# Kernel tuning notes

Hardware: AMD Instinct MI355X
Metric: run time of the kernel (lower is better)

Reference implementation:

```python
import jax, jax.numpy as jnp
import numpy as np

NL, DM, DI, DS, DR, DC = 4, 1024, 2048, 16, 64, 4
B, L, DLOC, NC = 8, 224, 672, 10
EPS = 1e-5


def _rmsnorm(h, w):
    return h * jax.lax.rsqrt(jnp.mean(h * h, axis=-1, keepdims=True) + EPS) * w


def setup_inputs() -> dict:
    key = jax.random.key(0)
    ks = jax.random.split(key, 10)
    s = 0.02
    return dict(
        x=jax.random.normal(ks[0], (B, L, DLOC), jnp.float32),
        w_proj=jax.random.normal(ks[1], (DLOC, DM), jnp.float32) * s,
        b_proj=jnp.zeros((DM,), jnp.float32),
        norm_w=jnp.ones((NL, DM), jnp.float32),
        w_in=jax.random.normal(ks[2], (NL, DM, 2 * DI), jnp.float32) * s,
        w_conv=jax.random.normal(ks[3], (NL, DI, DC), jnp.float32) * s,
        b_conv=jnp.zeros((NL, DI), jnp.float32),
        w_x=jax.random.normal(ks[4], (NL, DI, DR + 2 * DS), jnp.float32) * s,
        w_dt=jax.random.normal(ks[5], (NL, DR, DI), jnp.float32) * s,
        b_dt=jax.random.normal(ks[6], (NL, DI), jnp.float32) * 0.1,
        A_log=jnp.broadcast_to(jnp.log(jnp.arange(1, DS + 1, dtype=jnp.float32)), (NL, DI, DS)) + jnp.zeros((NL, DI, DS), jnp.float32),
        Dp=jnp.ones((NL, DI), jnp.float32),
        w_out=jax.random.normal(ks[7], (NL, DI, DM), jnp.float32) * s,
        final_norm_w=jnp.ones((DM,), jnp.float32),
        w_fc=jax.random.normal(ks[8], (DM, NC), jnp.float32) * s,
        b_fc=jnp.zeros((NC,), jnp.float32),
    )


def reference(x, w_proj, b_proj, norm_w, w_in, w_conv, b_conv, w_x, w_dt, b_dt, A_log, Dp, w_out, final_norm_w, w_fc, b_fc):
    # input_proj: (B,L,DLOC) -> (B,L,DM)
    h = x @ w_proj + b_proj
    for l in range(NL):
        xn = _rmsnorm(h, norm_w[l])
        xz = xn @ w_in[l]                      # (B,L,2*DI)
        xp, z = jnp.split(xz, 2, axis=-1)
        # causal depthwise conv1d along L, kernel size DC
        xpad = jnp.pad(xp, ((0, 0), (DC - 1, 0), (0, 0)))
        xc = sum(xpad[:, k:k + L, :] * w_conv[l][:, k] for k in range(DC)) + b_conv[l]
        xc = jax.nn.silu(xc)
        x_dbl = xc @ w_x[l]                    # (B,L,DR+2*DS)
        dtr, Bm, Cm = jnp.split(x_dbl, [DR, DR + DS], axis=-1)
        dt = jax.nn.softplus(dtr @ w_dt[l] + b_dt[l])   # (B,L,DI)
        A = -jnp.exp(A_log[l])                 # (DI,DS)
        xs = (jnp.swapaxes(dt, 0, 1), jnp.swapaxes(Bm, 0, 1),
              jnp.swapaxes(Cm, 0, 1), jnp.swapaxes(xc, 0, 1))

        def step(hs, inp):
            dt_t, B_t, C_t, u_t = inp          # (B,DI),(B,DS),(B,DS),(B,DI)
            dA = jnp.exp(dt_t[:, :, None] * A)                        # (B,DI,DS)
            hs = dA * hs + (dt_t * u_t)[:, :, None] * B_t[:, None, :]
            y = jnp.einsum('bds,bs->bd', hs, C_t)
            return hs, y

        h0 = jnp.zeros((B, DI, DS), x.dtype)
        _, ys = jax.lax.scan(step, h0, xs)     # ys: (L,B,DI)
        y = jnp.swapaxes(ys, 0, 1) + Dp[l] * xc
        y = y * jax.nn.silu(z)
        h = h + y @ w_out[l]
    h = _rmsnorm(h, final_norm_w)
    pooled = h[:, -1, :]                       # last-token pooling
    return pooled @ w_fc + b_fc                # (B,NC)
```

## Files before the change

### kernel.cpp

```cpp
#include <hip/hip_runtime.h>
#include <hip/hip_bf16.h>
#include <hip/hip_fp16.h>
#include <math.h>

#define NL 4
#define DM 1024
#define DI 2048
#define DS 16
#define DR 64
#define DC 4
#define B_ 8
#define L_ 224
#define DLOC 672
#define NC 10
#define EPS 1e-5f

#define ROWS (B_ * L_)

typedef unsigned short u16;
typedef __attribute__((ext_vector_type(8))) short bf16x8;
typedef __attribute__((ext_vector_type(4))) float f32x4;
typedef __attribute__((address_space(1))) const void gvoid_t;
typedef __attribute__((address_space(3))) void lvoid_t;

__device__ __forceinline__ u16 f2bf(float f) {
  union { float f; unsigned int u; } v;
  v.f = f;
  unsigned int u = v.u;
  return (u16)((u + 0x7fffu + ((u >> 16) & 1u)) >> 16);
}

__device__ __forceinline__ void load4h(const __half* p, float* o) {
  uint2 r = *(const uint2*)p;
  __half2 h0 = *(__half2*)&r.x;
  __half2 h1 = *(__half2*)&r.y;
  float2 f0 = __half22float2(h0);
  float2 f1 = __half22float2(h1);
  o[0] = f0.x; o[1] = f0.y; o[2] = f1.x; o[3] = f1.y;
}

__device__ __forceinline__ void load8h(const __half* p, float* o) {
  uint4 r = *(const uint4*)p;
  __half2 h0 = *(__half2*)&r.x;
  __half2 h1 = *(__half2*)&r.y;
  __half2 h2 = *(__half2*)&r.z;
  __half2 h3 = *(__half2*)&r.w;
  float2 f0 = __half22float2(h0);
  float2 f1 = __half22float2(h1);
  float2 f2 = __half22float2(h2);
  float2 f3 = __half22float2(h3);
  o[0] = f0.x; o[1] = f0.y; o[2] = f1.x; o[3] = f1.y;
  o[4] = f2.x; o[5] = f2.y; o[6] = f3.x; o[7] = f3.y;
}

template <int ACC, int BIAS, int TSTORE>
__global__ __launch_bounds__(256) void gemm_bt_mfma(
    const u16* __restrict__ A, const u16* __restrict__ Bt,
    const float* __restrict__ bias, float* __restrict__ C, int K, int lda,
    int ldb, int ldc) {
  __shared__ __align__(16) u16 As[128 * 32];
  __shared__ __align__(16) u16 Bs[128 * 32];
  const int tid = threadIdx.x;
  const int lane = tid & 63;
  const int wv = tid >> 6;
  const int n0 = blockIdx.x * 128;
  const int m0 = blockIdx.y * 128;
  const int wm0 = (wv & 1) * 64;
  const int wn0 = (wv >> 1) * 64;
  const int quad = lane >> 4;
  const int l16 = lane & 15;

  const int srow = wv * 32 + (lane >> 2);
  const int scol = (lane & 3) * 8;
  const u16* ga0 = A + (size_t)(m0 + srow) * lda + scol;
  const u16* ga1 = ga0 + (size_t)16 * lda;
  const u16* gb0 = Bt + (size_t)(n0 + srow) * ldb + scol;
  const u16* gb1 = gb0 + (size_t)16 * ldb;
  u16* la0 = &As[(wv * 32) * 32];
  u16* la1 = &As[(wv * 32 + 16) * 32];
  u16* lb0 = &Bs[(wv * 32) * 32];
  u16* lb1 = &Bs[(wv * 32 + 16) * 32];

  f32x4 acc[4][4] = {};

  for (int k0 = 0; k0 < K; k0 += 32) {
    __syncthreads();
    __builtin_amdgcn_global_load_lds((gvoid_t*)ga0, (lvoid_t*)la0, 16, 0, 0);
    __builtin_amdgcn_global_load_lds((gvoid_t*)ga1, (lvoid_t*)la1, 16, 0, 0);
    __builtin_amdgcn_global_load_lds((gvoid_t*)gb0, (lvoid_t*)lb0, 16, 0, 0);
    __builtin_amdgcn_global_load_lds((gvoid_t*)gb1, (lvoid_t*)lb1, 16, 0, 0);
    __syncthreads();
    bf16x8 af[4], bfr[4];
#pragma unroll
    for (int i = 0; i < 4; i++)
      af[i] = *(const bf16x8*)&As[(wm0 + i * 16 + l16) * 32 + quad * 8];
#pragma unroll
    for (int j = 0; j < 4; j++)
      bfr[j] = *(const bf16x8*)&Bs[(wn0 + j * 16 + l16) * 32 + quad * 8];
#pragma unroll
    for (int i = 0; i < 4; i++)
#pragma unroll
      for (int j = 0; j < 4; j++)
        acc[i][j] = __builtin_amdgcn_mfma_f32_16x16x32_bf16(af[i], bfr[j],
                                                            acc[i][j], 0, 0, 0);
    ga0 += 32; ga1 += 32; gb0 += 32; gb1 += 32;
  }

#pragma unroll
  for (int i = 0; i < 4; i++) {
#pragma unroll
    for (int j = 0; j < 4; j++) {
      const int col = n0 + wn0 + j * 16 + l16;
      const int rowb = m0 + wm0 + i * 16 + quad * 4;
      if (TSTORE) {
        __half* Ch = (__half*)C;
        __half2 p0, p1;
        p0.x = __float2half(acc[i][j][0]); p0.y = __float2half(acc[i][j][1]);
        p1.x = __float2half(acc[i][j][2]); p1.y = __float2half(acc[i][j][3]);
        union { __half2 h[2]; uint2 u; } pk;
        pk.h[0] = p0; pk.h[1] = p1;
        *(uint2*)(Ch + (size_t)col * ldc + rowb) = pk.u;
      } else {
        float bv = 0.f;
        if (BIAS) bv = bias[col];
#pragma unroll
        for (int r = 0; r < 4; r++) {
          float v = acc[i][j][r] + bv;
          float* p = C + (size_t)(rowb + r) * ldc + col;
          if (ACC) v += *p;
          *p = v;
        }
      }
    }
  }
}

template <int ACC, int ACT, int SPLITK, int BROW, typename BT, typename OT>
__global__ __launch_bounds__(256) void gemm_kernel(
    const float* __restrict__ A, const BT* __restrict__ Bm,
    const float* __restrict__ bias, OT* __restrict__ C, int M, int N, int K,
    int lda, int ldb, int ldc) {
  if (SPLITK) {
    A += (size_t)blockIdx.z * 256;
    Bm += (size_t)blockIdx.z * 256 * ldb;
  }
  __shared__ float As[16][64];
  __shared__ float Bs[16][64];
  const int tid = threadIdx.x;
  const int tx = tid & 15;
  const int ty = tid >> 4;
  const int n0 = blockIdx.x * 64;
  const int m0 = blockIdx.y * 64;
  const int am = tid & 63;
  const int ak = (tid >> 6) * 4;
  const int bk = tid >> 4;
  const int bn = (tid & 15) * 4;

  float acc[4][4];
#pragma unroll
  for (int i = 0; i < 4; i++)
#pragma unroll
    for (int j = 0; j < 4; j++) acc[i][j] = 0.f;

  for (int k0 = 0; k0 < K; k0 += 16) {
    float4 av = *(const float4*)(A + (size_t)(m0 + am) * lda + k0 + ak);
    float4 bv;
    {
      int n = n0 + bn;
      const BT* bp = Bm + (size_t)(k0 + bk) * ldb + n;
      if (n + 3 < N) {
        if (sizeof(BT) == 2) {
          load4h((const __half*)bp, (float*)&bv);
        } else {
          bv = *(const float4*)(const void*)bp;
        }
      } else {
        bv.x = (n + 0 < N) ? (float)bp[0] : 0.f;
        bv.y = (n + 1 < N) ? (float)bp[1] : 0.f;
        bv.z = (n + 2 < N) ? (float)bp[2] : 0.f;
        bv.w = (n + 3 < N) ? (float)bp[3] : 0.f;
      }
    }
    __syncthreads();
    As[ak + 0][am] = av.x;
    As[ak + 1][am] = av.y;
    As[ak + 2][am] = av.z;
    As[ak + 3][am] = av.w;
    *(float4*)(&Bs[bk][bn]) = bv;
    __syncthreads();
#pragma unroll
    for (int kk = 0; kk < 16; kk++) {
      float4 a4 = *(const float4*)(&As[kk][ty * 4]);
      float4 b4 = *(const float4*)(&Bs[kk][tx * 4]);
      float ar[4] = {a4.x, a4.y, a4.z, a4.w};
      float br[4] = {b4.x, b4.y, b4.z, b4.w};
#pragma unroll
      for (int i = 0; i < 4; i++)
#pragma unroll
        for (int j = 0; j < 4; j++) acc[i][j] = fmaf(ar[i], br[j], acc[i][j]);
    }
  }

#pragma unroll
  for (int i = 0; i < 4; i++) {
    int m = m0 + ty * 4 + i;
#pragma unroll
    for (int j = 0; j < 4; j++) {
      int n = n0 + tx * 4 + j;
      if (n < N && m < M) {
        float v = acc[i][j];
        if (BROW == 2) v += bias[m];
        if (ACT == 1) v = (v > 20.f) ? v : log1pf(expf(v));
        OT* p = C + (size_t)m * ldc + n;
        if (ACC == 2) {
          atomicAdd((float*)p, v);
        } else {
          *p = (OT)v;
        }
      }
    }
  }
}

__global__ __launch_bounds__(256) void transpose_cvt_kernel(
    const float* __restrict__ src, u16* __restrict__ dst, int K, int N) {
  __shared__ float t[32][33];
  const int n0 = blockIdx.x * 32;
  const int k0 = blockIdx.y * 32;
  const int c = threadIdx.x & 31;
  const int r = threadIdx.x >> 5;
#pragma unroll
  for (int rr = 0; rr < 4; rr++)
    t[r + rr * 8][c] = src[(size_t)(k0 + r + rr * 8) * N + n0 + c];
  __syncthreads();
#pragma unroll
  for (int rr = 0; rr < 4; rr++)
    dst[(size_t)(n0 + r + rr * 8) * K + k0 + c] = f2bf(t[c][r + rr * 8]);
}

__global__ __launch_bounds__(256) void transpose_f32_kernel(
    const float* __restrict__ src, float* __restrict__ dst, int K, int N) {
  __shared__ float t[32][33];
  const int n0 = blockIdx.x * 32;
  const int k0 = blockIdx.y * 32;
  const int c = threadIdx.x & 31;
  const int r = threadIdx.x >> 5;
#pragma unroll
  for (int rr = 0; rr < 4; rr++)
    t[r + rr * 8][c] = src[(size_t)(k0 + r + rr * 8) * N + n0 + c];
  __syncthreads();
#pragma unroll
  for (int rr = 0; rr < 4; rr++)
    dst[(size_t)(n0 + r + rr * 8) * K + k0 + c] = t[c][r + rr * 8];
}

__global__ __launch_bounds__(256) void transpose_u16_kernel(
    const u16* __restrict__ src, u16* __restrict__ dst, int K, int N) {
  __shared__ u16 t[32][33];
  const int n0 = blockIdx.x * 32;
  const int k0 = blockIdx.y * 32;
  const int c = threadIdx.x & 31;
  const int r = threadIdx.x >> 5;
#pragma unroll
  for (int rr = 0; rr < 4; rr++)
    t[r + rr * 8][c] = src[(size_t)(k0 + r + rr * 8) * N + n0 + c];
  __syncthreads();
#pragma unroll
  for (int rr = 0; rr < 4; rr++)
    dst[(size_t)(n0 + r + rr * 8) * K + k0 + c] = t[c][r + rr * 8];
}

__global__ __launch_bounds__(256) void cvt_kernel(const float* __restrict__ src,
                                                  u16* __restrict__ dst) {
  const int i = blockIdx.x * 256 + threadIdx.x;
  const float4 v = ((const float4*)src)[i];
  ushort4 o;
  o.x = f2bf(v.x);
  o.y = f2bf(v.y);
  o.z = f2bf(v.z);
  o.w = f2bf(v.w);
  ((ushort4*)dst)[i] = o;
}

__global__ __launch_bounds__(256) void rmsnorm_kernel(
    const float* __restrict__ h, const float* __restrict__ w,
    u16* __restrict__ out) {
  const int row = blockIdx.x;
  const int tid = threadIdx.x;
  const float4 v = *(const float4*)(h + (size_t)row * DM + tid * 4);
  float ss = v.x * v.x + v.y * v.y + v.z * v.z + v.w * v.w;
#pragma unroll
  for (int off = 32; off > 0; off >>= 1) ss += __shfl_xor(ss, off);
  __shared__ float red[4];
  if ((tid & 63) == 0) red[tid >> 6] = ss;
  __syncthreads();
  float tot = red[0] + red[1] + red[2] + red[3];
  const float inv = rsqrtf(tot / (float)DM + EPS);
  const float4 wv = *(const float4*)(w + tid * 4);
  ushort4 o;
  o.x = f2bf(v.x * inv * wv.x);
  o.y = f2bf(v.y * inv * wv.y);
  o.z = f2bf(v.z * inv * wv.z);
  o.w = f2bf(v.w * inv * wv.w);
  *(ushort4*)(out + (size_t)row * DM + tid * 4) = o;
}

__global__ __launch_bounds__(256) void conv_silu_t_kernel(
    const __half* __restrict__ xpT, const float* __restrict__ wc,
    const float* __restrict__ bc, __half* __restrict__ uT) {
  const int idx = blockIdx.x * 256 + threadIdx.x;
  const int d = idx / (ROWS / 4);
  const int r4 = (idx - d * (ROWS / 4)) * 4;
  const int t0 = r4 % L_;
  const __half* row = xpT + (size_t)d * ROWS + r4;
  float v[4];
  load4h(row, v);
  float p0 = 0.f, p1 = 0.f, p2 = 0.f;
  if (t0 > 0) {
    p0 = __half2float(row[-3]);
    p1 = __half2float(row[-2]);
    p2 = __half2float(row[-1]);
  }
  const float w0 = wc[d * 4 + 0], w1 = wc[d * 4 + 1], w2 = wc[d * 4 + 2],
              w3 = wc[d * 4 + 3];
  const float bb = bc[d];
  float o[4];
  float s;
  s = bb + p0 * w0 + p1 * w1 + p2 * w2 + v[0] * w3; o[0] = s / (1.f + expf(-s));
  s = bb + p1 * w0 + p2 * w1 + v[0] * w2 + v[1] * w3; o[1] = s / (1.f + expf(-s));
  s = bb + p2 * w0 + v[0] * w1 + v[1] * w2 + v[2] * w3; o[2] = s / (1.f + expf(-s));
  s = bb + v[0] * w0 + v[1] * w1 + v[2] * w2 + v[3] * w3; o[3] = s / (1.f + expf(-s));
  union { __half2 h[2]; uint2 u; } pk;
  pk.h[0].x = __float2half(o[0]); pk.h[0].y = __float2half(o[1]);
  pk.h[1].x = __float2half(o[2]); pk.h[1].y = __float2half(o[3]);
  *(uint2*)(uT + (size_t)d * ROWS + r4) = pk.u;
}

__global__ __launch_bounds__(256) void scan_kernel(
    const __half* __restrict__ dtT, const __half* __restrict__ uT,
    const __half* __restrict__ zT, const float* __restrict__ xdblT,
    const float* __restrict__ A_log, const float* __restrict__ Dp,
    u16* __restrict__ yT) {
  __shared__ __align__(16) __half dtu[4][2][512];
  __shared__ __align__(16) __half zbuf[4][2][512];
  __shared__ __align__(16) float bcb[2][32 * 36];

  const int tid = threadIdx.x;
  const int wv = tid >> 6;
  const int lane = tid & 63;
  const int b = blockIdx.x >> 6;
  const int d0 = ((blockIdx.x & 63) << 5) + wv * 8;
  const int c = lane >> 3;
  const int sg = lane & 7;
  const int d = d0 + c;
  const int s0 = sg * 2;

  const int sl = lane & 31;
  const size_t srcoff =
      (size_t)(d0 + (sl & 7)) * ROWS + (size_t)b * L_ + (sl >> 3) * 8;
  const __half* gdtu = (lane < 32 ? dtT : uT) + srcoff;
  const __half* gz = zT + srcoff;

  const int bs = tid >> 3;
  const int bt4 = (tid & 7) * 4;
  const float* gbc = xdblT + (size_t)(DR + bs) * ROWS + (size_t)b * L_ + bt4;

  const float2 Al = *(const float2*)(A_log + (size_t)d * DS + s0);
  const float A20 = -expf(Al.x) * 1.44269504f;
  const float A21 = -expf(Al.y) * 1.44269504f;
  const float Dpd = Dp[d];
  u16* yp = yT + (size_t)d * ROWS + b * L_;

  float hs0 = 0.f, hs1 = 0.f;

  auto stage_dtuz = [&](int t0, int p) {
    __builtin_amdgcn_global_load_lds((gvoid_t*)(gdtu + t0),
                                     (lvoid_t*)&dtu[wv][p][0], 16, 0, 0);
    __builtin_amdgcn_global_load_lds((gvoid_t*)(gz + t0),
                                     (lvoid_t*)&zbuf[wv][p][0], 16, 0, 0);
  };

  {
    float4 bc0 = *(const float4*)gbc;
    stage_dtuz(0, 0);
    __builtin_amdgcn_s_waitcnt(0x0f70);
    *(float4*)&bcb[0][bs * 36 + bt4] = bc0;
    __syncthreads();
  }

  for (int ch = 0; ch < L_ / 32; ch++) {
    const int p = ch & 1;
    const int t0 = ch * 32;
    float4 bcn;
    const bool more = (ch + 1 < L_ / 32);
    if (more) {
      bcn = *(const float4*)(gbc + t0 + 32);
      stage_dtuz(t0 + 32, p ^ 1);
    }
#pragma unroll
    for (int g = 0; g < 4; g++) {
      float dt8[8], u8[8], z8[8];
      load8h(&dtu[wv][p][g * 64 + c * 8], dt8);
      load8h(&dtu[wv][p][256 + g * 64 + c * 8], u8);
      load8h(&zbuf[wv][p][g * 64 + c * 8], z8);
      union { u16 h[8]; uint4 v; } yb;
#pragma unroll
      for (int k = 0; k < 8; k++) {
        const int tt = g * 8 + k;
        const float Bv0 = bcb[p][s0 * 36 + tt];
        const float Bv1 = bcb[p][(s0 + 1) * 36 + tt];
        const float Cv0 = bcb[p][(16 + s0) * 36 + tt];
        const float Cv1 = bcb[p][(17 + s0) * 36 + tt];
        const float dtv = dt8[k];
        const float uu = u8[k];
        const float du = dtv * uu;
        hs0 = fmaf(hs0, exp2f(dtv * A20), du * Bv0);
        hs1 = fmaf(hs1, exp2f(dtv * A21), du * Bv1);
        float pr = fmaf(hs1, Cv1, hs0 * Cv0);
        pr += __shfl_xor(pr, 1);
        pr += __shfl_xor(pr, 2);
        pr += __shfl_xor(pr, 4);
        if (sg == 0) {
          const float zz = z8[k];
          float yv = pr + Dpd * uu;
          yv *= zz / (1.f + expf(-zz));
          yb.h[k] = f2bf(yv);
        }
      }
      if (sg == 0) *(uint4*)(yp + t0 + g * 8) = yb.v;
    }
    if (more) {
      __builtin_amdgcn_s_waitcnt(0x0f70);
      *(float4*)&bcb[p ^ 1][bs * 36 + bt4] = bcn;
    }
    __syncthreads();
  }
}

__global__ __launch_bounds__(256) void final_kernel(
    const float* __restrict__ h, const float* __restrict__ fnw,
    const float* __restrict__ w_fc, const float* __restrict__ b_fc,
    float* __restrict__ out) {
  const int b = blockIdx.x;
  const int tid = threadIdx.x;
  const size_t row = ((size_t)b * L_ + (L_ - 1)) * DM;
  const float4 v = *(const float4*)(h + row + tid * 4);
  float ss = v.x * v.x + v.y * v.y + v.z * v.z + v.w * v.w;
#pragma unroll
  for (int off = 32; off > 0; off >>= 1) ss += __shfl_xor(ss, off);
  __shared__ float red[4];
  if ((tid & 63) == 0) red[tid >> 6] = ss;
  __syncthreads();
  float tot = red[0] + red[1] + red[2] + red[3];
  const float inv = rsqrtf(tot / (float)DM + EPS);
  const float4 wv = *(const float4*)(fnw + tid * 4);
  float hn[4] = {v.x * inv * wv.x, v.y * inv * wv.y, v.z * inv * wv.z,
                 v.w * inv * wv.w};
  float partial[NC];
#pragma unroll
  for (int j = 0; j < NC; j++) partial[j] = 0.f;
#pragma unroll
  for (int e = 0; e < 4; e++) {
    const int dd = tid * 4 + e;
#pragma unroll
    for (int j = 0; j < NC; j++)
      partial[j] = fmaf(hn[e], w_fc[dd * NC + j], partial[j]);
  }
  __shared__ float red2[256][NC];
  for (int j = 0; j < NC; j++) red2[tid][j] = partial[j];
  __syncthreads();
  for (int stride = 128; stride > 0; stride >>= 1) {
    if (tid < stride)
      for (int j = 0; j < NC; j++) red2[tid][j] += red2[tid + stride][j];
    __syncthreads();
  }
  if (tid < NC) out[b * NC + tid] = red2[0][tid] + b_fc[tid];
}

extern "C" void kernel_launch(void* const* d_in, const int* in_sizes, int n_in,
                              void* d_out, int out_size, void* d_ws,
                              size_t ws_size, hipStream_t stream) {
  const float* x = (const float*)d_in[0];
  const float* w_proj = (const float*)d_in[1];
  const float* b_proj = (const float*)d_in[2];
  const float* norm_w = (const float*)d_in[3];
  const float* w_in = (const float*)d_in[4];
  const float* w_conv = (const float*)d_in[5];
  const float* b_conv = (const float*)d_in[6];
  const float* w_x = (const float*)d_in[7];
  const float* w_dt = (const float*)d_in[8];
  const float* b_dt = (const float*)d_in[9];
  const float* A_log = (const float*)d_in[10];
  const float* Dp = (const float*)d_in[11];
  const float* w_out = (const float*)d_in[12];
  const float* fnw = (const float*)d_in[13];
  const float* w_fc = (const float*)d_in[14];
  const float* b_fc = (const float*)d_in[15];
  float* out = (float*)d_out;

  float* ws = (float*)d_ws;
  float* h = ws;
  __half* xzT = (__half*)(h + 1835008);
  __half* uT = (__half*)(h + 1835008 + 3670016);
  float* xdblT = h + 1835008 + 3670016 + 1835008;
  __half* dtT = (__half*)(xdblT + 172032);
  float* nxt = xdblT + 172032 + 1835008;
  u16* yT = (u16*)nxt;
  u16* y16 = (u16*)(nxt + 1835008);
  u16* xn16 = y16;
  u16* x16 = (u16*)(nxt + 3670016);
  u16* wprojT = (u16*)(nxt + 4272128);
  u16* winT = (u16*)(nxt + 4616192);
  u16* woutT = (u16*)(nxt + 6713344);
  float* w_xT = nxt + 7761920;
  float* w_dtT = w_xT + 196608;

  const dim3 blk(256);

  cvt_kernel<<<ROWS * DLOC / 1024, blk, 0, stream>>>(x, x16);
  transpose_cvt_kernel<<<dim3(DM / 32, DLOC / 32), blk, 0, stream>>>(
      w_proj, wprojT, DLOC, DM);

  gemm_bt_mfma<0, 1, 0><<<dim3(DM / 128, ROWS / 128), blk, 0, stream>>>(
      x16, wprojT, b_proj, h, DLOC, DLOC, DLOC, DM);

  for (int l = 0; l < NL; l++) {
    transpose_cvt_kernel<<<dim3(2 * DI / 32, DM / 32), blk, 0, stream>>>(
        w_in + (size_t)l * DM * 2 * DI, winT, DM, 2 * DI);
    transpose_cvt_kernel<<<dim3(DM / 32, DI / 32), blk, 0, stream>>>(
        w_out + (size_t)l * DI * DM, woutT, DI, DM);
    transpose_f32_kernel<<<dim3(96 / 32, DI / 32), blk, 0, stream>>>(
        w_x + (size_t)l * DI * 96, w_xT, DI, 96);
    transpose_f32_kernel<<<dim3(DI / 32, DR / 32), blk, 0, stream>>>(
        w_dt + (size_t)l * DR * DI, w_dtT, DR, DI);

    rmsnorm_kernel<<<ROWS, blk, 0, stream>>>(h, norm_w + (size_t)l * DM, xn16);
    gemm_bt_mfma<0, 0, 1><<<dim3(2 * DI / 128, ROWS / 128), blk, 0, stream>>>(
        xn16, winT, nullptr, (float*)xzT, DM, DM, DM, ROWS);
    conv_silu_t_kernel<<<DI * (ROWS / 4) / 256, blk, 0, stream>>>(
        xzT, w_conv + (size_t)l * DI * DC, b_conv + (size_t)l * DI, uT);
    hipMemsetAsync(xdblT, 0, (size_t)96 * ROWS * sizeof(float), stream);
    gemm_kernel<2, 0, 1, 0, __half, float>
        <<<dim3(ROWS / 64, 2, 8), blk, 0, stream>>>(
            w_xT, uT, nullptr, xdblT, 96, ROWS, 256, DI, ROWS, ROWS);
    gemm_kernel<0, 1, 0, 2, float, __half>
        <<<dim3(ROWS / 64, DI / 64), blk, 0, stream>>>(
            w_dtT, xdblT, b_dt + (size_t)l * DI, dtT, DI, ROWS, DR, DR, ROWS,
            ROWS);
    scan_kernel<<<dim3(B_ * (DI / 32)), blk, 0, stream>>>(
        dtT, uT, xzT + (size_t)DI * ROWS, xdblT, A_log + (size_t)l * DI * DS,
        Dp + (size_t)l * DI, yT);
    transpose_u16_kernel<<<dim3(ROWS / 32, DI / 32), blk, 0, stream>>>(
        yT, y16, DI, ROWS);
    gemm_bt_mfma<1, 0, 0><<<dim3(DM / 128, ROWS / 128), blk, 0, stream>>>(
        y16, woutT, nullptr, h, DI, DI, DI, DM);
  }

  final_kernel<<<B_, blk, 0, stream>>>(h, fnw, w_fc, b_fc, out);
}
```

Baseline: 1.144 ms.

## Move x_proj and dt_proj GEMMs to bf16 MFMA and fuse weight prep

Replaces the scalar fp32 GEMMs for x_proj (split-K with atomics) and dt_proj with the bf16 MFMA GEMM, which gains split-K, row-bias, softplus and half-output variants. The conv/silu kernel now also writes a row-major bf16 copy of u through an LDS tile, and a transpose produces a bf16 dtr operand. The four per-layer weight transpose launches are merged into one prep kernel, and the scan loads B/C coefficients as vectors. Running these projections in bf16 lowers their precision and needs padding of the 96-wide x_dbl to 128 rows, plus extra transpose passes.

```diff
diff --git a/kernel.cpp b/kernel.cpp
--- a/kernel.cpp
+++ b/kernel.cpp
@@ -53,11 +53,15 @@
   o[4] = f2.x; o[5] = f2.y; o[6] = f3.x; o[7] = f3.y;
 }
 
-template <int ACC, int BIAS, int TSTORE>
+template <int ACC, int BROW, int TSTORE, int ACT, int SPLITK, typename OT>
 __global__ __launch_bounds__(256) void gemm_bt_mfma(
     const u16* __restrict__ A, const u16* __restrict__ Bt,
-    const float* __restrict__ bias, float* __restrict__ C, int K, int lda,
+    const float* __restrict__ bias, OT* __restrict__ C, int K, int lda,
     int ldb, int ldc) {
+  if (SPLITK) {
+    A += (size_t)blockIdx.z * SPLITK;
+    Bt += (size_t)blockIdx.z * SPLITK;
+  }
   __shared__ __align__(16) u16 As[128 * 32];
   __shared__ __align__(16) u16 Bs[128 * 32];
   const int tid = threadIdx.x;
@@ -114,121 +118,41 @@
       const int rowb = m0 + wm0 + i * 16 + quad * 4;
       if (TSTORE) {
         __half* Ch = (__half*)C;
-        __half2 p0, p1;
-        p0.x = __float2half(acc[i][j][0]); p0.y = __float2half(acc[i][j][1]);
-        p1.x = __float2half(acc[i][j][2]); p1.y = __float2half(acc[i][j][3]);
         union { __half2 h[2]; uint2 u; } pk;
-        pk.h[0] = p0; pk.h[1] = p1;
+        pk.h[0].x = __float2half(acc[i][j][0]);
+        pk.h[0].y = __float2half(acc[i][j][1]);
+        pk.h[1].x = __float2half(acc[i][j][2]);
+        pk.h[1].y = __float2half(acc[i][j][3]);
         *(uint2*)(Ch + (size_t)col * ldc + rowb) = pk.u;
       } else {
         float bv = 0.f;
-        if (BIAS) bv = bias[col];
+        if (BROW == 1) bv = bias[col];
 #pragma unroll
         for (int r = 0; r < 4; r++) {
           float v = acc[i][j][r] + bv;
-          float* p = C + (size_t)(rowb + r) * ldc + col;
-          if (ACC) v += *p;
-          *p = v;
+          if (BROW == 2) v += bias[rowb + r];
+          if (ACT == 1) v = (v > 20.f) ? v : log1pf(expf(v));
+          OT* p = C + (size_t)(rowb + r) * ldc + col;
+          if (ACC == 2) {
+            atomicAdd((float*)p, v);
+          } else {
+            if (ACC == 1) v += (float)*p;
+            *p = (OT)v;
+          }
         }
       }
     }
   }
 }
 
-template <int ACC, int ACT, int SPLITK, int BROW, typename BT, typename OT>
-__global__ __launch_bounds__(256) void gemm_kernel(
-    const float* __restrict__ A, const BT* __restrict__ Bm,
-    const float* __restrict__ bias, OT* __restrict__ C, int M, int N, int K,
-    int lda, int ldb, int ldc) {
-  if (SPLITK) {
-    A += (size_t)blockIdx.z * 256;
-    Bm += (size_t)blockIdx.z * 256 * ldb;
-  }
-  __shared__ float As[16][64];
-  __shared__ float Bs[16][64];
-  const int tid = threadIdx.x;
-  const int tx = tid & 15;
-  const int ty = tid >> 4;
-  const int n0 = blockIdx.x * 64;
-  const int m0 = blockIdx.y * 64;
-  const int am = tid & 63;
-  const int ak = (tid >> 6) * 4;
-  const int bk = tid >> 4;
-  const int bn = (tid & 15) * 4;
-
-  float acc[4][4];
-#pragma unroll
-  for (int i = 0; i < 4; i++)
-#pragma unroll
-    for (int j = 0; j < 4; j++) acc[i][j] = 0.f;
-
-  for (int k0 = 0; k0 < K; k0 += 16) {
-    float4 av = *(const float4*)(A + (size_t)(m0 + am) * lda + k0 + ak);
-    float4 bv;
-    {
-      int n = n0 + bn;
-      const BT* bp = Bm + (size_t)(k0 + bk) * ldb + n;
-      if (n + 3 < N) {
-        if (sizeof(BT) == 2) {
-          load4h((const __half*)bp, (float*)&bv);
-        } else {
-          bv = *(const float4*)(const void*)bp;
-        }
-      } else {
-        bv.x = (n + 0 < N) ? (float)bp[0] : 0.f;
-        bv.y = (n + 1 < N) ? (float)bp[1] : 0.f;
-        bv.z = (n + 2 < N) ? (float)bp[2] : 0.f;
-        bv.w = (n + 3 < N) ? (float)bp[3] : 0.f;
-      }
-    }
-    __syncthreads();
-    As[ak + 0][am] = av.x;
-    As[ak + 1][am] = av.y;
-    As[ak + 2][am] = av.z;
-    As[ak + 3][am] = av.w;
-    *(float4*)(&Bs[bk][bn]) = bv;
-    __syncthreads();
-#pragma unroll
-    for (int kk = 0; kk < 16; kk++) {
-      float4 a4 = *(const float4*)(&As[kk][ty * 4]);
-      float4 b4 = *(const float4*)(&Bs[kk][tx * 4]);
-      float ar[4] = {a4.x, a4.y, a4.z, a4.w};
-      float br[4] = {b4.x, b4.y, b4.z, b4.w};
-#pragma unroll
-      for (int i = 0; i < 4; i++)
-#pragma unroll
-        for (int j = 0; j < 4; j++) acc[i][j] = fmaf(ar[i], br[j], acc[i][j]);
-    }
-  }
-
-#pragma unroll
-  for (int i = 0; i < 4; i++) {
-    int m = m0 + ty * 4 + i;
-#pragma unroll
-    for (int j = 0; j < 4; j++) {
-      int n = n0 + tx * 4 + j;
-      if (n < N && m < M) {
-        float v = acc[i][j];
-        if (BROW == 2) v += bias[m];
-        if (ACT == 1) v = (v > 20.f) ? v : log1pf(expf(v));
-        OT* p = C + (size_t)m * ldc + n;
-        if (ACC == 2) {
-          atomicAdd((float*)p, v);
-        } else {
-          *p = (OT)v;
-        }
-      }
-    }
-  }
-}
-
-__global__ __launch_bounds__(256) void transpose_cvt_kernel(
-    const float* __restrict__ src, u16* __restrict__ dst, int K, int N) {
+__device__ __forceinline__ void transpose_cvt_body(
+    const float* __restrict__ src, u16* __restrict__ dst, int K, int N,
+    int bx, int by, int tid) {
   __shared__ float t[32][33];
-  const int n0 = blockIdx.x * 32;
-  const int k0 = blockIdx.y * 32;
-  const int c = threadIdx.x & 31;
-  const int r = threadIdx.x >> 5;
+  const int n0 = bx * 32;
+  const int k0 = by * 32;
+  const int c = tid & 31;
+  const int r = tid >> 5;
 #pragma unroll
   for (int rr = 0; rr < 4; rr++)
     t[r + rr * 8][c] = src[(size_t)(k0 + r + rr * 8) * N + n0 + c];
@@ -238,20 +162,32 @@
     dst[(size_t)(n0 + r + rr * 8) * K + k0 + c] = f2bf(t[c][r + rr * 8]);
 }
 
-__global__ __launch_bounds__(256) void transpose_f32_kernel(
-    const float* __restrict__ src, float* __restrict__ dst, int K, int N) {
-  __shared__ float t[32][33];
-  const int n0 = blockIdx.x * 32;
-  const int k0 = blockIdx.y * 32;
-  const int c = threadIdx.x & 31;
-  const int r = threadIdx.x >> 5;
-#pragma unroll
-  for (int rr = 0; rr < 4; rr++)
-    t[r + rr * 8][c] = src[(size_t)(k0 + r + rr * 8) * N + n0 + c];
-  __syncthreads();
-#pragma unroll
-  for (int rr = 0; rr < 4; rr++)
-    dst[(size_t)(n0 + r + rr * 8) * K + k0 + c] = t[c][r + rr * 8];
+__global__ __launch_bounds__(256) void transpose_cvt_kernel(
+    const float* __restrict__ src, u16* __restrict__ dst, int K, int N) {
+  transpose_cvt_body(src, dst, K, N, blockIdx.x, blockIdx.y, threadIdx.x);
+}
+
+__global__ __launch_bounds__(256) void prep_weights_kernel(
+    const float* __restrict__ w_in_l, const float* __restrict__ w_out_l,
+    const float* __restrict__ w_x_l, const float* __restrict__ w_dt_l,
+    u16* __restrict__ winT, u16* __restrict__ woutT, u16* __restrict__ w_x16,
+    u16* __restrict__ w_dt16) {
+  int bid = blockIdx.x;
+  if (bid < 4096) {
+    transpose_cvt_body(w_in_l, winT, DM, 2 * DI, bid & 127, bid >> 7,
+                       threadIdx.x);
+  } else if (bid < 6144) {
+    bid -= 4096;
+    transpose_cvt_body(w_out_l, woutT, DI, DM, bid & 31, bid >> 5,
+                       threadIdx.x);
+  } else if (bid < 6336) {
+    bid -= 6144;
+    transpose_cvt_body(w_x_l, w_x16, DI, 96, bid % 3, bid / 3, threadIdx.x);
+  } else {
+    bid -= 6336;
+    transpose_cvt_body(w_dt_l, w_dt16, DR, DI, bid & 63, bid >> 6,
+                       threadIdx.x);
+  }
 }
 
 __global__ __launch_bounds__(256) void transpose_u16_kernel(
@@ -305,18 +241,24 @@
   *(ushort4*)(out + (size_t)row * DM + tid * 4) = o;
 }
 
-__global__ __launch_bounds__(256) void conv_silu_t_kernel(
+__global__ __launch_bounds__(256) void conv_silu_tile_kernel(
     const __half* __restrict__ xpT, const float* __restrict__ wc,
-    const float* __restrict__ bc, __half* __restrict__ uT) {
-  const int idx = blockIdx.x * 256 + threadIdx.x;
-  const int d = idx / (ROWS / 4);
-  const int r4 = (idx - d * (ROWS / 4)) * 4;
-  const int t0 = r4 % L_;
-  const __half* row = xpT + (size_t)d * ROWS + r4;
+    const float* __restrict__ bc, __half* __restrict__ uT,
+    u16* __restrict__ u16rm) {
+  __shared__ u16 tile[32][33];
+  const int tid = threadIdx.x;
+  const int d0 = blockIdx.x * 32;
+  const int r0 = blockIdx.y * 32;
+  const int dl = tid >> 3;
+  const int rq = (tid & 7) * 4;
+  const int d = d0 + dl;
+  const int r = r0 + rq;
+  const int t = r % L_;
+  const __half* row = xpT + (size_t)d * ROWS + r;
   float v[4];
   load4h(row, v);
   float p0 = 0.f, p1 = 0.f, p2 = 0.f;
-  if (t0 > 0) {
+  if (t > 0) {
     p0 = __half2float(row[-3]);
     p1 = __half2float(row[-2]);
     p2 = __half2float(row[-1]);
@@ -333,7 +275,18 @@
   union { __half2 h[2]; uint2 u; } pk;
   pk.h[0].x = __float2half(o[0]); pk.h[0].y = __float2half(o[1]);
   pk.h[1].x = __float2half(o[2]); pk.h[1].y = __float2half(o[3]);
-  *(uint2*)(uT + (size_t)d * ROWS + r4) = pk.u;
+  *(uint2*)(uT + (size_t)d * ROWS + r) = pk.u;
+#pragma unroll
+  for (int i = 0; i < 4; i++) tile[rq + i][dl] = f2bf(o[i]);
+  __syncthreads();
+  const int rl = tid >> 3;
+  const int dq = (tid & 7) * 4;
+  ushort4 ov;
+  ov.x = tile[rl][dq + 0];
+  ov.y = tile[rl][dq + 1];
+  ov.z = tile[rl][dq + 2];
+  ov.w = tile[rl][dq + 3];
+  *(ushort4*)(u16rm + (size_t)(r0 + rl) * DI + d0 + dq) = ov;
 }
 
 __global__ __launch_bounds__(256) void scan_kernel(
@@ -403,20 +356,24 @@
       load8h(&dtu[wv][p][g * 64 + c * 8], dt8);
       load8h(&dtu[wv][p][256 + g * 64 + c * 8], u8);
       load8h(&zbuf[wv][p][g * 64 + c * 8], z8);
+      float Bv0[8], Bv1[8], Cv0[8], Cv1[8];
+      *(float4*)&Bv0[0] = *(const float4*)&bcb[p][s0 * 36 + g * 8];
+      *(float4*)&Bv0[4] = *(const float4*)&bcb[p][s0 * 36 + g * 8 + 4];
+      *(float4*)&Bv1[0] = *(const float4*)&bcb[p][(s0 + 1) * 36 + g * 8];
+      *(float4*)&Bv1[4] = *(const float4*)&bcb[p][(s0 + 1) * 36 + g * 8 + 4];
+      *(float4*)&Cv0[0] = *(const float4*)&bcb[p][(16 + s0) * 36 + g * 8];
+      *(float4*)&Cv0[4] = *(const float4*)&bcb[p][(16 + s0) * 36 + g * 8 + 4];
+      *(float4*)&Cv1[0] = *(const float4*)&bcb[p][(17 + s0) * 36 + g * 8];
+      *(float4*)&Cv1[4] = *(const float4*)&bcb[p][(17 + s0) * 36 + g * 8 + 4];
       union { u16 h[8]; uint4 v; } yb;
 #pragma unroll
       for (int k = 0; k < 8; k++) {
-        const int tt = g * 8 + k;
-        const float Bv0 = bcb[p][s0 * 36 + tt];
-        const float Bv1 = bcb[p][(s0 + 1) * 36 + tt];
-        const float Cv0 = bcb[p][(16 + s0) * 36 + tt];
-        const float Cv1 = bcb[p][(17 + s0) * 36 + tt];
         const float dtv = dt8[k];
         const float uu = u8[k];
         const float du = dtv * uu;
-        hs0 = fmaf(hs0, exp2f(dtv * A20), du * Bv0);
-        hs1 = fmaf(hs1, exp2f(dtv * A21), du * Bv1);
-        float pr = fmaf(hs1, Cv1, hs0 * Cv0);
+        hs0 = fmaf(hs0, exp2f(dtv * A20), du * Bv0[k]);
+        hs1 = fmaf(hs1, exp2f(dtv * A21), du * Bv1[k]);
+        float pr = fmaf(hs1, Cv1[k], hs0 * Cv0[k]);
         pr += __shfl_xor(pr, 1);
         pr += __shfl_xor(pr, 2);
         pr += __shfl_xor(pr, 4);
@@ -500,20 +457,35 @@
 
   float* ws = (float*)d_ws;
   float* h = ws;
-  __half* xzT = (__half*)(h + 1835008);
-  __half* uT = (__half*)(h + 1835008 + 3670016);
-  float* xdblT = h + 1835008 + 3670016 + 1835008;
-  __half* dtT = (__half*)(xdblT + 172032);
-  float* nxt = xdblT + 172032 + 1835008;
-  u16* yT = (u16*)nxt;
-  u16* y16 = (u16*)(nxt + 1835008);
+  float* p1 = h + 1835008;
+  __half* xzT = (__half*)p1;
+  float* p2 = p1 + 3670016;
+  __half* uT = (__half*)p2;
+  float* p3 = p2 + 1835008;
+  float* xdblT = p3;
+  float* p4 = p3 + 229376;
+  __half* dtT = (__half*)p4;
+  float* p5 = p4 + 1835008;
+  u16* yT = (u16*)p5;
+  float* p6 = p5 + 1835008;
+  u16* y16 = (u16*)p6;
   u16* xn16 = y16;
-  u16* x16 = (u16*)(nxt + 3670016);
-  u16* wprojT = (u16*)(nxt + 4272128);
-  u16* winT = (u16*)(nxt + 4616192);
-  u16* woutT = (u16*)(nxt + 6713344);
-  float* w_xT = nxt + 7761920;
-  float* w_dtT = w_xT + 196608;
+  float* p7 = p6 + 1835008;
+  u16* u16rm = (u16*)p7;
+  float* p8 = p7 + 1835008;
+  u16* x16 = (u16*)p8;
+  float* p9 = p8 + 602112;
+  u16* wprojT = (u16*)p9;
+  float* p10 = p9 + 344064;
+  u16* winT = (u16*)p10;
+  float* p11 = p10 + 2097152;
+  u16* woutT = (u16*)p11;
+  float* p12 = p11 + 1048576;
+  u16* w_x16 = (u16*)p12;
+  float* p13 = p12 + 131072;
+  u16* w_dt16 = (u16*)p13;
+  float* p14 = p13 + 65536;
+  u16* dtr16 = (u16*)p14;
 
   const dim3 blk(256);
 
@@ -521,39 +493,39 @@
   transpose_cvt_kernel<<<dim3(DM / 32, DLOC / 32), blk, 0, stream>>>(
       w_proj, wprojT, DLOC, DM);
 
-  gemm_bt_mfma<0, 1, 0><<<dim3(DM / 128, ROWS / 128), blk, 0, stream>>>(
-      x16, wprojT, b_proj, h, DLOC, DLOC, DLOC, DM);
+  gemm_bt_mfma<0, 1, 0, 0, 0, float>
+      <<<dim3(DM / 128, ROWS / 128), blk, 0, stream>>>(
+          x16, wprojT, b_proj, h, DLOC, DLOC, DLOC, DM);
 
   for (int l = 0; l < NL; l++) {
-    transpose_cvt_kernel<<<dim3(2 * DI / 32, DM / 32), blk, 0, stream>>>(
-        w_in + (size_t)l * DM * 2 * DI, winT, DM, 2 * DI);
-    transpose_cvt_kernel<<<dim3(DM / 32, DI / 32), blk, 0, stream>>>(
-        w_out + (size_t)l * DI * DM, woutT, DI, DM);
-    transpose_f32_kernel<<<dim3(96 / 32, DI / 32), blk, 0, stream>>>(
-        w_x + (size_t)l * DI * 96, w_xT, DI, 96);
-    transpose_f32_kernel<<<dim3(DI / 32, DR / 32), blk, 0, stream>>>(
-        w_dt + (size_t)l * DR * DI, w_dtT, DR, DI);
+    prep_weights_kernel<<<6464, blk, 0, stream>>>(
+        w_in + (size_t)l * DM * 2 * DI, w_out + (size_t)l * DI * DM,
+        w_x + (size_t)l * DI * 96, w_dt + (size_t)l * DR * DI, winT, woutT,
+        w_x16, w_dt16);
 
     rmsnorm_kernel<<<ROWS, blk, 0, stream>>>(h, norm_w + (size_t)l * DM, xn16);
-    gemm_bt_mfma<0, 0, 1><<<dim3(2 * DI / 128, ROWS / 128), blk, 0, stream>>>(
-        xn16, winT, nullptr, (float*)xzT, DM, DM, DM, ROWS);
-    conv_silu_t_kernel<<<DI * (ROWS / 4) / 256, blk, 0, stream>>>(
-        xzT, w_conv + (size_t)l * DI * DC, b_conv + (size_t)l * DI, uT);
-    hipMemsetAsync(xdblT, 0, (size_t)96 * ROWS * sizeof(float), stream);
-    gemm_kernel<2, 0, 1, 0, __half, float>
-        <<<dim3(ROWS / 64, 2, 8), blk, 0, stream>>>(
-            w_xT, uT, nullptr, xdblT, 96, ROWS, 256, DI, ROWS, ROWS);
-    gemm_kernel<0, 1, 0, 2, float, __half>
-        <<<dim3(ROWS / 64, DI / 64), blk, 0, stream>>>(
-            w_dtT, xdblT, b_dt + (size_t)l * DI, dtT, DI, ROWS, DR, DR, ROWS,
-            ROWS);
+    gemm_bt_mfma<0, 0, 1, 0, 0, __half>
+        <<<dim3(2 * DI / 128, ROWS / 128), blk, 0, stream>>>(
+            xn16, winT, nullptr, (__half*)xzT, DM, DM, DM, ROWS);
+    conv_silu_tile_kernel<<<dim3(DI / 32, ROWS / 32), blk, 0, stream>>>(
+        xzT, w_conv + (size_t)l * DI * DC, b_conv + (size_t)l * DI, uT, u16rm);
+    hipMemsetAsync(xdblT, 0, (size_t)128 * ROWS * sizeof(float), stream);
+    gemm_bt_mfma<2, 0, 0, 0, 512, float>
+        <<<dim3(ROWS / 128, 1, 4), blk, 0, stream>>>(
+            w_x16, u16rm, nullptr, xdblT, 512, DI, DI, ROWS);
+    transpose_cvt_kernel<<<dim3(ROWS / 32, DR / 32), blk, 0, stream>>>(
+        xdblT, dtr16, DR, ROWS);
+    gemm_bt_mfma<0, 2, 0, 1, 0, __half>
+        <<<dim3(ROWS / 128, DI / 128), blk, 0, stream>>>(
+            w_dt16, dtr16, b_dt + (size_t)l * DI, dtT, DR, DR, DR, ROWS);
     scan_kernel<<<dim3(B_ * (DI / 32)), blk, 0, stream>>>(
         dtT, uT, xzT + (size_t)DI * ROWS, xdblT, A_log + (size_t)l * DI * DS,
         Dp + (size_t)l * DI, yT);
     transpose_u16_kernel<<<dim3(ROWS / 32, DI / 32), blk, 0, stream>>>(
         yT, y16, DI, ROWS);
-    gemm_bt_mfma<1, 0, 0><<<dim3(DM / 128, ROWS / 128), blk, 0, stream>>>(
-        y16, woutT, nullptr, h, DI, DI, DI, DM);
+    gemm_bt_mfma<1, 0, 0, 0, 0, float>
+        <<<dim3(DM / 128, ROWS / 128), blk, 0, stream>>>(
+            y16, woutT, nullptr, h, DI, DI, DI, DM);
   }
 
   final_kernel<<<B_, blk, 0, stream>>>(h, fnw, w_fc, b_fc, out);
```

After: 1.073 ms. -6.2%, faster.
